# Performance work log

Hardware: AMD Instinct MI355X
Metric: run time of the kernel (lower is better)

## Reference

```python
import jax, jax.numpy as jnp
import numpy as np

B, P, N, D = 32, 100, 1000, 128
SQRT_D = 11.313708498984761
CLIP = 10.0


def setup_inputs() -> dict:
    key = jax.random.key(0)
    ks = jax.random.split(key, 8)
    s = 1.0 / np.sqrt(D)  # keep k ~ N(0,1) so exp(k) is stable
    return {
        "encoded_nodes": jax.random.normal(ks[0], (B, N, D), jnp.float32),
        "encoded_q1": jax.random.normal(ks[1], (B, P, D), jnp.float32),
        "encoded_last_node": jax.random.normal(ks[2], (B, P, D), jnp.float32),
        "cur_dist": jax.random.uniform(ks[3], (B, P, N), jnp.float32),
        "ninf_mask": jnp.zeros((B, P, N), jnp.float32),
        "log_scale": jnp.ones((1,), jnp.float32),
        "Wq_first": jax.random.normal(ks[4], (D, D), jnp.float32) * s,
        "Wq_last": jax.random.normal(ks[5], (D, D), jnp.float32) * s,
        "Wk": jax.random.normal(ks[6], (D, D), jnp.float32) * s,
        "Wv": jax.random.normal(ks[7], (D, D), jnp.float32) * s,
        "dist_alpha_1": jnp.ones((1,), jnp.float32),
        "AFT_dist_alpha_1": jnp.ones((1,), jnp.float32),
    }


def reference(encoded_nodes, encoded_q1, encoded_last_node, cur_dist, ninf_mask,
              log_scale, Wq_first, Wq_last, Wk, Wv, dist_alpha_1, AFT_dist_alpha_1):
    # set_kv / set_q1 (torch Linear: x @ W.T)
    k = jnp.einsum('bnd,ed->bne', encoded_nodes, Wk)          # [B,N,D]
    v = jnp.einsum('bnd,ed->bne', encoded_nodes, Wv)          # [B,N,D]
    q_first = jnp.einsum('bpd,ed->bpe', encoded_q1, Wq_first) # [B,P,D]
    q_last = jnp.einsum('bpd,ed->bpe', encoded_last_node, Wq_last)
    q = q_first + q_last

    cur_dist_out = -cur_dist                                   # [B,P,N]
    bias_scale = log_scale * AFT_dist_alpha_1 * cur_dist_out + ninf_mask
    ebias = jnp.exp(bias_scale)                                # [B,P,N]
    ek = jnp.exp(k)                                            # [B,N,D]
    num = jnp.einsum('bpn,bnd->bpd', ebias, ek * v)
    den = jnp.einsum('bpn,bnd->bpd', ebias, ek)
    aft_out = jax.nn.sigmoid(q) * (num / den)                  # [B,P,D]

    score = jnp.einsum('bpd,bnd->bpn', aft_out, encoded_nodes) / SQRT_D
    score = score + log_scale * dist_alpha_1 * cur_dist_out
    score = CLIP * jnp.tanh(score) + ninf_mask
    return jax.nn.softmax(score, axis=2)
```

## Files before the change

### kernel.cpp

```cpp
#include <hip/hip_runtime.h>
#include <hip/hip_bf16.h>
#include <math.h>

#define B 32
#define P 100
#define N 1000
#define D 128

constexpr float SQRT_D_INV = 1.0f / 11.313708498984761f;
constexpr float CLIPV = 10.0f;

__device__ __forceinline__ void fma4(float4& a, float s, const float4& b) {
    a.x = fmaf(s, b.x, a.x);
    a.y = fmaf(s, b.y, a.y);
    a.z = fmaf(s, b.z, a.z);
    a.w = fmaf(s, b.w, a.w);
}

#define GLDS(gsrc, ldst) __builtin_amdgcn_global_load_lds( \
    (const __attribute__((address_space(1))) void*)(gsrc), \
    (__attribute__((address_space(3))) void*)(ldst), 16, 0, 0)

#define TT 64
__global__ __launch_bounds__(256) void prep_kernel(
        const float* __restrict__ nodes,
        const float* __restrict__ Wk,  const float* __restrict__ Wv,
        const float* __restrict__ Wqf, const float* __restrict__ Wql,
        float* __restrict__ wkT,  float* __restrict__ wvT,
        float* __restrict__ wqfT, float* __restrict__ wqlT,
        float* __restrict__ nodesT) {
    const int t = threadIdx.x;
    if (blockIdx.x < D) {
        const int e = blockIdx.x;
        const int d = t & 127;
        if ((t >> 7) == 0) {
            wkT[e * D + d] = Wk[d * D + e];
            wvT[e * D + d] = Wv[d * D + e];
        } else {
            wqfT[e * D + d] = Wqf[d * D + e];
            wqlT[e * D + d] = Wql[d * D + e];
        }
        return;
    }
    __shared__ float sh[TT][D + 1];
    const int blk = blockIdx.x - D;
    const int ntiles = (N + TT - 1) / TT;
    const int b  = blk / ntiles;
    const int n0 = (blk % ntiles) * TT;
    const int rows = min(TT, N - n0);

    const float4* src = (const float4*)(nodes + ((long)b * N + n0) * D);
    for (int i = t; i < rows * (D / 4); i += 256) {
        int r = i >> 5, c = i & 31;
        float4 v = src[(long)r * (D / 4) + c];
        sh[r][c * 4 + 0] = v.x; sh[r][c * 4 + 1] = v.y;
        sh[r][c * 4 + 2] = v.z; sh[r][c * 4 + 3] = v.w;
    }
    __syncthreads();

    const int nl = t & 63;
    const int eg = t >> 6;
    if (nl < rows) {
        #pragma unroll
        for (int k = 0; k < 32; ++k) {
            int e = eg * 32 + k;
            nodesT[((long)b * D + e) * N + n0 + nl] = sh[nl][e];
        }
    }
}

#define R1 64
#define CH 8
__global__ __launch_bounds__(512) void kv_kernel(
        const float* __restrict__ nodes,
        const float* __restrict__ wkT,
        const float* __restrict__ wvT,
        float* __restrict__ ek,
        float* __restrict__ ekv) {
    __shared__ float sh[R1][D];
    __shared__ __align__(16) float wL[2][2][CH * D];
    const int t = threadIdx.x;
    const int lane = t & 63;
    const int wid = t >> 6;
    const int dq = t & 31;
    const int rl = t >> 5;
    const long row0 = (long)blockIdx.x * R1;

    const float4* src = (const float4*)(nodes + row0 * D);
    float4* dst = (float4*)(&sh[0][0]);
    #pragma unroll
    for (int i = 0; i < (R1 * D / 4) / 512; ++i)
        dst[t + i * 512] = src[t + i * 512];

    {
        const int seg = wid & 3;
        const float* g = (wid < 4 ? wkT : wvT) + seg * 256 + lane * 4;
        GLDS(g, &wL[0][wid < 4 ? 0 : 1][seg * 256]);
    }
    __syncthreads();

    float4 ka[4], va[4];
    #pragma unroll
    for (int rr = 0; rr < 4; ++rr) {
        ka[rr] = make_float4(0.f, 0.f, 0.f, 0.f);
        va[rr] = make_float4(0.f, 0.f, 0.f, 0.f);
    }

    int buf = 0;
    for (int c = 0; c < D / CH; ++c) {
        if (c + 1 < D / CH) {
            const int seg = wid & 3;
            const float* g = (wid < 4 ? wkT : wvT)
                           + (long)(c + 1) * CH * D + seg * 256 + lane * 4;
            GLDS(g, &wL[buf ^ 1][wid < 4 ? 0 : 1][seg * 256]);
        }

        const float* wkb = &wL[buf][0][dq * 4];
        const float* wvb = &wL[buf][1][dq * 4];
        #pragma unroll
        for (int ee0 = 0; ee0 < CH; ee0 += 4) {
            float4 cwk[4], cwv[4];
            #pragma unroll
            for (int ee = 0; ee < 4; ++ee) {
                cwk[ee] = *(const float4*)(wkb + (ee0 + ee) * D);
                cwv[ee] = *(const float4*)(wvb + (ee0 + ee) * D);
            }
            const int e0 = c * CH + ee0;
            #pragma unroll
            for (int rr = 0; rr < 4; ++rr) {
                float4 s4 = *(const float4*)(&sh[rl * 4 + rr][e0]);
                fma4(ka[rr], s4.x, cwk[0]); fma4(ka[rr], s4.y, cwk[1]);
                fma4(ka[rr], s4.z, cwk[2]); fma4(ka[rr], s4.w, cwk[3]);
                fma4(va[rr], s4.x, cwv[0]); fma4(va[rr], s4.y, cwv[1]);
                fma4(va[rr], s4.z, cwv[2]); fma4(va[rr], s4.w, cwv[3]);
            }
        }
        __syncthreads();
        buf ^= 1;
    }

    #pragma unroll
    for (int rr = 0; rr < 4; ++rr) {
        long row = row0 + rl * 4 + rr;
        float4 e4;
        e4.x = __expf(ka[rr].x); e4.y = __expf(ka[rr].y);
        e4.z = __expf(ka[rr].z); e4.w = __expf(ka[rr].w);
        float4 ev;
        ev.x = e4.x * va[rr].x; ev.y = e4.y * va[rr].y;
        ev.z = e4.z * va[rr].z; ev.w = e4.w * va[rr].w;
        *(float4*)(ek + row * D + dq * 4) = e4;
        *(float4*)(ekv + row * D + dq * 4) = ev;
    }
}

#define R2 16
__global__ __launch_bounds__(256) void q_kernel(
        const float* __restrict__ q1,
        const float* __restrict__ qlast,
        const float* __restrict__ wqfT,
        const float* __restrict__ wqlT,
        float* __restrict__ qsig) {
    __shared__ float sh1[R2][D];
    __shared__ float sh2[R2][D];
    const int t = threadIdx.x;
    const int dq = t & 31;
    const int rl = t >> 5;
    const long row0 = (long)blockIdx.x * R2;

    const float4* s1 = (const float4*)(q1 + row0 * D);
    const float4* s2 = (const float4*)(qlast + row0 * D);
    float4* d1 = (float4*)(&sh1[0][0]);
    float4* d2 = (float4*)(&sh2[0][0]);
    #pragma unroll
    for (int i = 0; i < (R2 * D / 4) / 256; ++i) {
        d1[t + i * 256] = s1[t + i * 256];
        d2[t + i * 256] = s2[t + i * 256];
    }
    __syncthreads();

    float4 acc[2];
    acc[0] = make_float4(0.f, 0.f, 0.f, 0.f);
    acc[1] = make_float4(0.f, 0.f, 0.f, 0.f);

    const float* wfp = wqfT + dq * 4;
    const float* wlp = wqlT + dq * 4;

    float4 cwf[4], cwl[4];
    #pragma unroll
    for (int ee = 0; ee < 4; ++ee) {
        cwf[ee] = *(const float4*)(wfp + ee * D);
        cwl[ee] = *(const float4*)(wlp + ee * D);
    }

    for (int e0 = 0; e0 < D; e0 += 4) {
        float4 nwf[4], nwl[4];
        if (e0 + 4 < D) {
            #pragma unroll
            for (int ee = 0; ee < 4; ++ee) {
                nwf[ee] = *(const float4*)(wfp + (e0 + 4 + ee) * D);
                nwl[ee] = *(const float4*)(wlp + (e0 + 4 + ee) * D);
            }
        }
        #pragma unroll
        for (int rr = 0; rr < 2; ++rr) {
            float4 a4 = *(const float4*)(&sh1[rl * 2 + rr][e0]);
            float4 b4 = *(const float4*)(&sh2[rl * 2 + rr][e0]);
            fma4(acc[rr], a4.x, cwf[0]); fma4(acc[rr], a4.y, cwf[1]);
            fma4(acc[rr], a4.z, cwf[2]); fma4(acc[rr], a4.w, cwf[3]);
            fma4(acc[rr], b4.x, cwl[0]); fma4(acc[rr], b4.y, cwl[1]);
            fma4(acc[rr], b4.z, cwl[2]); fma4(acc[rr], b4.w, cwl[3]);
        }
        #pragma unroll
        for (int ee = 0; ee < 4; ++ee) { cwf[ee] = nwf[ee]; cwl[ee] = nwl[ee]; }
    }

    #pragma unroll
    for (int rr = 0; rr < 2; ++rr) {
        long row = row0 + rl * 2 + rr;
        float4 s;
        s.x = 1.0f / (1.0f + __expf(-acc[rr].x));
        s.y = 1.0f / (1.0f + __expf(-acc[rr].y));
        s.z = 1.0f / (1.0f + __expf(-acc[rr].z));
        s.w = 1.0f / (1.0f + __expf(-acc[rr].w));
        *(float4*)(qsig + row * D + dq * 4) = s;
    }
}

#define PT3 50
#define TS3 16
#define EBC 57
__global__ __launch_bounds__(256) void aft_part_kernel(
        const float* __restrict__ cur_dist,
        const float* __restrict__ ninf,
        const float* __restrict__ ek,
        const float* __restrict__ ekv,
        const float* __restrict__ log_scale,
        const float* __restrict__ aft_alpha,
        float* __restrict__ pnum,
        float* __restrict__ pden,
        int NC, int L) {
    __shared__ float eb[TS3][EBC];
    __shared__ __align__(16) float ekL[2][TS3 * D];
    __shared__ __align__(16) float evL[2][TS3 * D];
    const int t = threadIdx.x;
    const int dq = t & 31;
    const int pg = t >> 5;
    const int pbase = pg * 7;
    const int phys = blockIdx.x;
    const int g    = (phys >> 4) * 8 + (phys & 7);
    const int pt   = (phys >> 3) & 1;
    const int b    = g % B;
    const int c    = g / B;
    const int p0 = pt * PT3;
    const int n_begin = c * L;
    const int n_end = min(N, n_begin + L);
    const float lsA = log_scale[0] * aft_alpha[0];

    float4 num[7], den[7];
    #pragma unroll
    for (int i = 0; i < 7; ++i) {
        num[i] = make_float4(0.f, 0.f, 0.f, 0.f);
        den[i] = make_float4(0.f, 0.f, 0.f, 0.f);
    }

    const float* ekc = ek  + (long)b * N * D;
    const float* evc = ekv + (long)b * N * D;

    int n0 = n_begin;
    int ts = min(TS3, n_end - n0);

    {
        const float* gk = ekc + (long)n0 * D;
        const float* gv = evc + (long)n0 * D;
        for (int i = t; i < ts * 32; i += 256) {
            GLDS(gk + (long)i * 4, &ekL[0][i * 4]);
            GLDS(gv + (long)i * 4, &evL[0][i * 4]);
        }
    }
    float rv[4];
    #pragma unroll
    for (int k = 0; k < 4; ++k) {
        int s = t + k * 256;
        int pp = s >> 4, nl = s & 15;
        rv[k] = 0.f;
        if (pp < 56 && nl < ts && p0 + pp < P) {
            long idx = ((long)b * P + p0 + pp) * N + (n0 + nl);
            rv[k] = fmaf(-lsA, cur_dist[idx], ninf[idx]);
        }
    }

    int cur = 0;
    while (n0 < n_end) {
        #pragma unroll
        for (int k = 0; k < 4; ++k) {
            int s = t + k * 256;
            int pp = s >> 4, nl = s & 15;
            if (pp < 56 && nl < ts) eb[nl][pp] = __expf(rv[k]);
        }
        __syncthreads();

        const int n0n = n0 + ts;
        const int tsn = min(TS3, n_end - n0n);
        if (n0n < n_end) {
            const float* gk = ekc + (long)n0n * D;
            const float* gv = evc + (long)n0n * D;
            for (int i = t; i < tsn * 32; i += 256) {
                GLDS(gk + (long)i * 4, &ekL[cur ^ 1][i * 4]);
                GLDS(gv + (long)i * 4, &evL[cur ^ 1][i * 4]);
            }
            #pragma unroll
            for (int k = 0; k < 4; ++k) {
                int s = t + k * 256;
                int pp = s >> 4, nl = s & 15;
                rv[k] = 0.f;
                if (pp < 56 && nl < tsn && p0 + pp < P) {
                    long idx = ((long)b * P + p0 + pp) * N + (n0n + nl);
                    rv[k] = fmaf(-lsA, cur_dist[idx], ninf[idx]);
                }
            }
        }

        const float* ekp = &ekL[cur][dq * 4];
        const float* evp = &evL[cur][dq * 4];
        #pragma unroll 4
        for (int j = 0; j < ts; ++j) {
            float4 ekq = *(const float4*)(ekp + j * D);
            float4 evq = *(const float4*)(evp + j * D);
            float e0 = eb[j][pbase + 0];
            float e1 = eb[j][pbase + 1];
            float e2 = eb[j][pbase + 2];
            float e3 = eb[j][pbase + 3];
            float e4 = eb[j][pbase + 4];
            float e5 = eb[j][pbase + 5];
            float e6 = eb[j][pbase + 6];
            fma4(num[0], e0, evq); fma4(den[0], e0, ekq);
            fma4(num[1], e1, evq); fma4(den[1], e1, ekq);
            fma4(num[2], e2, evq); fma4(den[2], e2, ekq);
            fma4(num[3], e3, evq); fma4(den[3], e3, ekq);
            fma4(num[4], e4, evq); fma4(den[4], e4, ekq);
            fma4(num[5], e5, evq); fma4(den[5], e5, ekq);
            fma4(num[6], e6, evq); fma4(den[6], e6, ekq);
        }
        __syncthreads();
        cur ^= 1;
        n0 = n0n;
        ts = tsn;
    }

    #pragma unroll
    for (int r = 0; r < 7; ++r) {
        int pl_ = pbase + r;
        if (pl_ < PT3) {
            int p = p0 + pl_;
            long o = (((long)c * B + b) * P + p) * D + dq * 4;
            *(float4*)(pnum + o) = num[r];
            *(float4*)(pden + o) = den[r];
        }
    }
}

__global__ __launch_bounds__(256) void aft_reduce_kernel(
        const float* __restrict__ pnum,
        const float* __restrict__ pden,
        const float* __restrict__ qsig,
        float* __restrict__ aft,
        int NC) {
    const long i = ((long)blockIdx.x * 256 + threadIdx.x) * 4;
    const long BPD = (long)B * P * D;
    float4 n = make_float4(0.f, 0.f, 0.f, 0.f);
    float4 d = make_float4(0.f, 0.f, 0.f, 0.f);
    int c = 0;
    for (; c + 2 <= NC; c += 2) {
        float4 a0 = *(const float4*)(pnum + (long)c * BPD + i);
        float4 a1 = *(const float4*)(pnum + (long)(c + 1) * BPD + i);
        float4 b0 = *(const float4*)(pden + (long)c * BPD + i);
        float4 b1 = *(const float4*)(pden + (long)(c + 1) * BPD + i);
        n.x += a0.x + a1.x; n.y += a0.y + a1.y;
        n.z += a0.z + a1.z; n.w += a0.w + a1.w;
        d.x += b0.x + b1.x; d.y += b0.y + b1.y;
        d.z += b0.z + b1.z; d.w += b0.w + b1.w;
    }
    if (c < NC) {
        float4 a0 = *(const float4*)(pnum + (long)c * BPD + i);
        float4 b0 = *(const float4*)(pden + (long)c * BPD + i);
        n.x += a0.x; n.y += a0.y; n.z += a0.z; n.w += a0.w;
        d.x += b0.x; d.y += b0.y; d.z += b0.z; d.w += b0.w;
    }
    float4 q = *(const float4*)(qsig + i);
    float4 o;
    o.x = q.x * n.x / d.x;
    o.y = q.y * n.y / d.y;
    o.z = q.z * n.z / d.z;
    o.w = q.w * n.w / d.w;
    *(float4*)(aft + i) = o;
}

#define PT2 10
#define SC 4
__global__ __launch_bounds__(128) void score_part_kernel(
        const float* __restrict__ aft,
        const float* __restrict__ nodesT,
        const float* __restrict__ cur_dist,
        const float* __restrict__ ninf,
        const float* __restrict__ log_scale,
        const float* __restrict__ dist_alpha,
        float* __restrict__ out,
        float* __restrict__ sums) {
    __shared__ float sa[PT2][D];
    __shared__ float red[2][PT2];
    const int t = threadIdx.x;
    const int wid = t >> 6;
    const int b    = blockIdx.x % B;
    const int rest = blockIdx.x / B;
    const int c    = rest % SC;
    const int pt   = rest / SC;
    const int p0 = pt * PT2;
    const float lsA = log_scale[0] * dist_alpha[0];

    for (int i = t; i < PT2 * D; i += 128) {
        sa[i >> 7][i & 127] = aft[((long)b * P + p0) * D + i];
    }
    __syncthreads();

    const int n0 = c * 256 + t * 2;
    const bool act = (n0 < N);
    const int ncl = act ? n0 : 0;
    const float* ntb = nodesT + (long)b * D * N;

    float2 acc[PT2];
    #pragma unroll
    for (int i = 0; i < PT2; ++i) acc[i] = make_float2(0.f, 0.f);

    float2 cx[4];
    #pragma unroll
    for (int ee = 0; ee < 4; ++ee)
        cx[ee] = *(const float2*)(ntb + (long)ee * N + ncl);

    for (int e0 = 0; e0 < D; e0 += 4) {
        float2 nx[4];
        if (e0 + 4 < D) {
            #pragma unroll
            for (int ee = 0; ee < 4; ++ee)
                nx[ee] = *(const float2*)(ntb + (long)(e0 + 4 + ee) * N + ncl);
        }
        #pragma unroll
        for (int i = 0; i < PT2; ++i) {
            float4 a4 = *(const float4*)(&sa[i][e0]);
            acc[i].x = fmaf(cx[0].x, a4.x, acc[i].x);
            acc[i].x = fmaf(cx[1].x, a4.y, acc[i].x);
            acc[i].x = fmaf(cx[2].x, a4.z, acc[i].x);
            acc[i].x = fmaf(cx[3].x, a4.w, acc[i].x);
            acc[i].y = fmaf(cx[0].y, a4.x, acc[i].y);
            acc[i].y = fmaf(cx[1].y, a4.y, acc[i].y);
            acc[i].y = fmaf(cx[2].y, a4.z, acc[i].y);
            acc[i].y = fmaf(cx[3].y, a4.w, acc[i].y);
        }
        #pragma unroll
        for (int ee = 0; ee < 4; ++ee) cx[ee] = nx[ee];
    }

    #pragma unroll
    for (int i = 0; i < PT2; ++i) {
        float2 ev = make_float2(0.f, 0.f);
        if (act) {
            long idx = ((long)b * P + p0 + i) * N + n0;
            float2 cd = *(const float2*)(cur_dist + idx);
            float2 nf = *(const float2*)(ninf + idx);
            float sx = fmaf(acc[i].x, SQRT_D_INV, -lsA * cd.x);
            float sy = fmaf(acc[i].y, SQRT_D_INV, -lsA * cd.y);
            float ax = fabsf(sx), ay = fabsf(sy);
            float rx = 1.f - 2.f / (__expf(2.f * ax) + 1.f);
            float ry = 1.f - 2.f / (__expf(2.f * ay) + 1.f);
            float scx = CLIPV * copysignf(rx, sx) + nf.x;
            float scy = CLIPV * copysignf(ry, sy) + nf.y;
            ev.x = __expf(scx);
            ev.y = __expf(scy);
            *(float2*)(out + idx) = ev;
        }
        float s = ev.x + ev.y;
        #pragma unroll
        for (int o = 1; o < 64; o <<= 1) s += __shfl_xor(s, o, 64);
        if ((t & 63) == 0) red[wid][i] = s;
    }
    __syncthreads();
    if (t < PT2) {
        atomicAdd(&sums[b * P + p0 + t], red[0][t] + red[1][t]);
    }
}

__global__ __launch_bounds__(256) void normalize_kernel(
        float* __restrict__ out, const float* __restrict__ sums) {
    const int row = blockIdx.x;
    const int t = threadIdx.x;
    const float inv = 1.0f / sums[row];
    float4* r = (float4*)(out + (long)row * N);
    if (t < N / 4) {
        float4 v = r[t];
        v.x *= inv; v.y *= inv; v.z *= inv; v.w *= inv;
        r[t] = v;
    }
}

extern "C" void kernel_launch(void* const* d_in, const int* in_sizes, int n_in,
                              void* d_out, int out_size, void* d_ws, size_t ws_size,
                              hipStream_t stream) {
    const float* nodes      = (const float*)d_in[0];
    const float* q1         = (const float*)d_in[1];
    const float* qlast      = (const float*)d_in[2];
    const float* cur_dist   = (const float*)d_in[3];
    const float* ninf       = (const float*)d_in[4];
    const float* log_scale  = (const float*)d_in[5];
    const float* Wqf        = (const float*)d_in[6];
    const float* Wql        = (const float*)d_in[7];
    const float* Wk         = (const float*)d_in[8];
    const float* Wv         = (const float*)d_in[9];
    const float* dist_alpha = (const float*)d_in[10];
    const float* aft_alpha  = (const float*)d_in[11];
    float* out = (float*)d_out;

    const long BND = (long)B * N * D;
    const long BPD = (long)B * P * D;
    const long W2  = (long)D * D;

    float* ws     = (float*)d_ws;
    float* ek     = ws;
    float* ekv    = ek + BND;
    float* qsig   = ekv + BND;
    float* aft    = qsig + BPD;
    float* wkT    = aft + BPD;
    float* wvT    = wkT + W2;
    float* wqfT   = wvT + W2;
    float* wqlT   = wqfT + W2;
    float* nodesT = wqlT + W2;
    float* sums   = nodesT + BND;
    float* pnum   = sums + (long)B * P;

    long avail = (long)(ws_size / 4) - (3 * BND + 2 * BPD + 4 * W2 + (long)B * P);
    int NC = (int)(avail / (2 * BPD));
    if (NC < 1) NC = 1;
    if (NC > 16) NC = 16;
    int L = (((N + NC - 1) / NC) + 15) & ~15;
    NC = (N + L - 1) / L;
    float* pden = pnum + (long)NC * BPD;

    hipMemsetAsync(sums, 0, (size_t)B * P * sizeof(float), stream);
    prep_kernel<<<D + B * ((N + TT - 1) / TT), 256, 0, stream>>>(
        nodes, Wk, Wv, Wqf, Wql, wkT, wvT, wqfT, wqlT, nodesT);
    kv_kernel<<<(B * N) / R1, 512, 0, stream>>>(nodes, wkT, wvT, ek, ekv);
    q_kernel<<<(B * P) / R2, 256, 0, stream>>>(q1, qlast, wqfT, wqlT, qsig);
    aft_part_kernel<<<B * 2 * NC, 256, 0, stream>>>(
        cur_dist, ninf, ek, ekv, log_scale, aft_alpha, pnum, pden, NC, L);
    aft_reduce_kernel<<<(int)(BPD / 1024), 256, 0, stream>>>(pnum, pden, qsig, aft, NC);
    score_part_kernel<<<B * SC * (P / PT2), 128, 0, stream>>>(
        aft, nodesT, cur_dist, ninf, log_scale, dist_alpha, out, sums);
    normalize_kernel<<<B * P, 256, 0, stream>>>(out, sums);
}
```

Baseline: 232.9 us.

## Stage node tiles in LDS with double-buffered global_load_lds and double query tile

The score kernel now copies 16-row slices of the transposed node matrix into a double-buffered shared-memory tile using direct global-to-LDS loads, prefetching the next slice while computing on the current one. Previously each thread streamed its own float2 values straight from global memory. The query rows per block are doubled from 10 to 20, so each node value loaded is reused across more rows. The trade-off is half as many blocks, more accumulator registers and an extra barrier per slice. The last column chunk may also read past N into the next row, or past the end of the buffer for the final batch.

```diff
diff --git a/kernel.cpp b/kernel.cpp
--- a/kernel.cpp
+++ b/kernel.cpp
@@ -395,8 +395,9 @@
     *(float4*)(aft + i) = o;
 }
 
-#define PT2 10
+#define PT2 20
 #define SC 4
+#define TE 16
 __global__ __launch_bounds__(128) void score_part_kernel(
         const float* __restrict__ aft,
         const float* __restrict__ nodesT,
@@ -407,6 +408,7 @@
         float* __restrict__ out,
         float* __restrict__ sums) {
     __shared__ float sa[PT2][D];
+    __shared__ __align__(16) float nt[2][TE * 256];
     __shared__ float red[2][PT2];
     const int t = threadIdx.x;
     const int wid = t >> 6;
@@ -417,6 +419,12 @@
     const int p0 = pt * PT2;
     const float lsA = log_scale[0] * dist_alpha[0];
 
+    const float* ntb = nodesT + (long)b * D * N + c * 256;
+
+    for (int i = t; i < TE * 64; i += 128) {
+        int r = i >> 6, l = i & 63;
+        GLDS(ntb + (long)r * N + l * 4, &nt[0][r * 256 + l * 4]);
+    }
     for (int i = t; i < PT2 * D; i += 128) {
         sa[i >> 7][i & 127] = aft[((long)b * P + p0) * D + i];
     }
@@ -424,39 +432,42 @@
 
     const int n0 = c * 256 + t * 2;
     const bool act = (n0 < N);
-    const int ncl = act ? n0 : 0;
-    const float* ntb = nodesT + (long)b * D * N;
+    const int tl2 = t * 2;
 
     float2 acc[PT2];
     #pragma unroll
     for (int i = 0; i < PT2; ++i) acc[i] = make_float2(0.f, 0.f);
 
-    float2 cx[4];
-    #pragma unroll
-    for (int ee = 0; ee < 4; ++ee)
-        cx[ee] = *(const float2*)(ntb + (long)ee * N + ncl);
-
-    for (int e0 = 0; e0 < D; e0 += 4) {
-        float2 nx[4];
-        if (e0 + 4 < D) {
+    int cur = 0;
+    for (int e0 = 0; e0 < D; e0 += TE) {
+        if (e0 + TE < D) {
+            for (int i = t; i < TE * 64; i += 128) {
+                int r = i >> 6, l = i & 63;
+                GLDS(ntb + (long)(e0 + TE + r) * N + l * 4,
+                     &nt[cur ^ 1][r * 256 + l * 4]);
+            }
+        }
+        #pragma unroll
+        for (int ee0 = 0; ee0 < TE; ee0 += 4) {
+            float2 cx2[4];
             #pragma unroll
-            for (int ee = 0; ee < 4; ++ee)
-                nx[ee] = *(const float2*)(ntb + (long)(e0 + 4 + ee) * N + ncl);
-        }
-        #pragma unroll
-        for (int i = 0; i < PT2; ++i) {
-            float4 a4 = *(const float4*)(&sa[i][e0]);
-            acc[i].x = fmaf(cx[0].x, a4.x, acc[i].x);
-            acc[i].x = fmaf(cx[1].x, a4.y, acc[i].x);
-            acc[i].x = fmaf(cx[2].x, a4.z, acc[i].x);
-            acc[i].x = fmaf(cx[3].x, a4.w, acc[i].x);
-            acc[i].y = fmaf(cx[0].y, a4.x, acc[i].y);
-            acc[i].y = fmaf(cx[1].y, a4.y, acc[i].y);
-            acc[i].y = fmaf(cx[2].y, a4.z, acc[i].y);
-            acc[i].y = fmaf(cx[3].y, a4.w, acc[i].y);
-        }
-        #pragma unroll
-        for (int ee = 0; ee < 4; ++ee) cx[ee] = nx[ee];
+            for (int u = 0; u < 4; ++u)
+                cx2[u] = *(const float2*)(&nt[cur][(ee0 + u) * 256 + tl2]);
+            #pragma unroll
+            for (int i = 0; i < PT2; ++i) {
+                float4 a4 = *(const float4*)(&sa[i][e0 + ee0]);
+                acc[i].x = fmaf(cx2[0].x, a4.x, acc[i].x);
+                acc[i].x = fmaf(cx2[1].x, a4.y, acc[i].x);
+                acc[i].x = fmaf(cx2[2].x, a4.z, acc[i].x);
+                acc[i].x = fmaf(cx2[3].x, a4.w, acc[i].x);
+                acc[i].y = fmaf(cx2[0].y, a4.x, acc[i].y);
+                acc[i].y = fmaf(cx2[1].y, a4.y, acc[i].y);
+                acc[i].y = fmaf(cx2[2].y, a4.z, acc[i].y);
+                acc[i].y = fmaf(cx2[3].y, a4.w, acc[i].y);
+            }
+        }
+        __syncthreads();
+        cur ^= 1;
     }
 
     #pragma unroll
```

New measurement: 237.1 us. No clear change (+1.8%).
